# Kernel optimization log

Hardware: AMD Instinct MI355X
Metric: run time of the kernel (lower is better)

## Reference

```python
import jax, jax.numpy as jnp
import numpy as np

N = 100000        # nodes
E = 3200000       # edges (avg in-degree ~32)
NG = 64           # graphs in batch
F_IN = 64         # num_node_features
AVG_LOG = float(np.log(33.0))   # avg log-degree baked from deg (avg degree 32)
BN_EPS = 1e-5
STD_EPS = 1e-5

def _glorot(key, fi, fo):
    lim = float(np.sqrt(6.0 / (fi + fo)))
    return jax.random.uniform(key, (fi, fo), jnp.float32, -lim, lim)

def setup_inputs():
    key = jax.random.key(0)
    ks = jax.random.split(key, 16)
    inp = {
        'x': jax.random.normal(ks[0], (N, F_IN), jnp.float32),
        'edge_index': jax.random.randint(ks[1], (2, E), 0, N),
        'batch': jnp.sort(jax.random.randint(ks[2], (N,), 0, NG)),
    }
    dims = [(F_IN, 96), (96, 64), (64, 32), (32, 20)]
    for i, (fi, fo) in enumerate(dims):
        inp[f'w{i}'] = _glorot(ks[3 + i], 13 * fi, fo)  # (4 aggr * 3 scalers + 1 self) * F_in
        inp[f'b{i}'] = jnp.zeros((fo,), jnp.float32)
    for i, c in enumerate([96, 64, 20]):
        inp[f'g{i}'] = jnp.ones((c,), jnp.float32)
        inp[f'be{i}'] = jnp.zeros((c,), jnp.float32)
    inp['w_lin'] = _glorot(ks[10], 20, 11)
    inp['b_lin'] = jnp.zeros((11,), jnp.float32)
    return inp

def _pna_layer(x, src, dst, cnt, degc, W, b):
    m = x[src]                                          # [E, F] gather of neighbor feats
    inv = (1.0 / degc)[:, None]
    mean = jax.ops.segment_sum(m, dst, N) * inv
    mean_sq = jax.ops.segment_sum(m * m, dst, N) * inv
    std = jnp.sqrt(jax.nn.relu(mean_sq - mean * mean) + STD_EPS)
    has = (cnt > 0)[:, None]
    mn = jnp.where(has, jax.ops.segment_min(m, dst, N), 0.0)
    mx = jnp.where(has, jax.ops.segment_max(m, dst, N), 0.0)
    agg = jnp.concatenate([mean, mn, mx, std], axis=-1)  # [N, 4F]
    logd = jnp.log(degc + 1.0)[:, None]
    out = jnp.concatenate([agg, agg * (logd / AVG_LOG), agg * (AVG_LOG / logd)], axis=-1)  # [N, 12F]
    out = jnp.concatenate([x, out], axis=-1)             # [N, 13F] self + scaled aggregations
    return out @ W + b

def _bn(x, g, b):
    mu = x.mean(0)
    var = x.var(0)  # biased var: matches torch BatchNorm training forward
    return (x - mu) * jax.lax.rsqrt(var + BN_EPS) * g + b

def _forward(x, edge_index, batch, w0, b0, w1, b1, w2, b2, w3, b3,
             g0, be0, g1, be1, g2, be2, w_lin, b_lin):
    src, dst = edge_index[0], edge_index[1]
    cnt = jax.ops.segment_sum(jnp.ones((E,), x.dtype), dst, N)  # in-degree
    degc = jnp.maximum(cnt, 1.0)
    h = jax.nn.relu(_bn(_pna_layer(x, src, dst, cnt, degc, w0, b0), g0, be0))
    h = jax.nn.relu(_bn(_pna_layer(h, src, dst, cnt, degc, w1, b1), g1, be1))
    h = jax.nn.relu(_pna_layer(h, src, dst, cnt, degc, w2, b2))
    h = _bn(_pna_layer(h, src, dst, cnt, degc, w3, b3), g2, be2)
    gcnt = jnp.maximum(jax.ops.segment_sum(jnp.ones((N,), h.dtype), batch, NG), 1.0)
    z = jax.ops.segment_sum(h, batch, NG) / gcnt[:, None]       # global mean pool [NG, 20]
    out = jax.nn.softmax(z @ w_lin + b_lin, axis=-1)            # dropout identity (eval)
    return out, z

def reference(x, edge_index, batch, w0, b0, w1, b1, w2, b2, w3, b3,
              g0, be0, g1, be1, g2, be2, w_lin, b_lin):
    return _forward(x, edge_index, batch, w0, b0, w1, b1, w2, b2, w3, b3,
                    g0, be0, g1, be1, g2, be2, w_lin, b_lin)
```

## Files before the change

### kernel.cpp

```cpp
#include <hip/hip_runtime.h>

#define NN 100000
#define NGRAPH 64
#define NPART 8
#define NPB 12500
#define DB 16
#define NSB 768
#define AVGLOG 3.4965075614664802f

using f32x4 = __attribute__((ext_vector_type(4))) float;
using f16x8 = __attribute__((ext_vector_type(8))) _Float16;
using f16x4 = __attribute__((ext_vector_type(4))) _Float16;

__global__ __launch_bounds__(256) void k_binstage(
    const int* __restrict__ ei, int* __restrict__ bcur,
    unsigned long long* __restrict__ bkt, int cap, int E) {
  __shared__ unsigned long long s_bkt[NPART][NSB];
  __shared__ int s_cnt[NPART], s_base[NPART];
  const int tid = threadIdx.x;
  const int lane = tid & 63;
  if (tid < NPART) s_cnt[tid] = 0;
  __syncthreads();
  const int total_ch = (E + 511) / 512;
  for (int ch = blockIdx.x; ch < total_ch; ch += gridDim.x) {
    int eA = ch * 512 + tid;
    int eB = eA + 256;
    int bA = -1, bB = -1;
    unsigned long long vA = 0, vB = 0;
    if (eA < E) {
      int d = __builtin_nontemporal_load(&ei[E + eA]);
      int s = __builtin_nontemporal_load(&ei[eA]);
      bA = d / NPB;
      vA = ((unsigned long long)(unsigned)d << 32) | (unsigned)s;
    }
    if (eB < E) {
      int d = __builtin_nontemporal_load(&ei[E + eB]);
      int s = __builtin_nontemporal_load(&ei[eB]);
      bB = d / NPB;
      vB = ((unsigned long long)(unsigned)d << 32) | (unsigned)s;
    }
#pragma unroll
    for (int b0 = 0; b0 < NPART; ++b0) {
      unsigned long long mA = __ballot(bA == b0);
      unsigned long long mB = __ballot(bB == b0);
      int cA = __popcll(mA);
      int tot = cA + __popcll(mB);
      if (tot) {
        int base = 0;
        if (lane == 0) base = atomicAdd(&s_cnt[b0], tot);
        base = __shfl(base, 0);
        if (bA == b0)
          s_bkt[b0][base + __popcll(mA & ((1ull << lane) - 1ull))] = vA;
        if (bB == b0)
          s_bkt[b0][base + cA + __popcll(mB & ((1ull << lane) - 1ull))] = vB;
      }
    }
    __syncthreads();
#pragma unroll
    for (int b0 = 0; b0 < NPART; ++b0) {
      int c = s_cnt[b0];
      int nfl = (c >= 512) ? (c & ~255) : 0;
      if (nfl) {
        if (tid == 0) s_base[b0] = atomicAdd(&bcur[b0], nfl);
        __syncthreads();
        int base = s_base[b0];
        for (int i = tid; i < nfl; i += 256)
          bkt[(size_t)b0 * cap + base + i] = s_bkt[b0][i];
        __syncthreads();
        int rem = c - nfl;
        if (tid < rem) s_bkt[b0][tid] = s_bkt[b0][nfl + tid];
        if (tid == 0) s_cnt[b0] = rem;
        __syncthreads();
      }
    }
  }
#pragma unroll
  for (int b0 = 0; b0 < NPART; ++b0) {
    int c = s_cnt[b0];
    if (c) {
      if (tid == 0) s_base[b0] = atomicAdd(&bcur[b0], c);
      __syncthreads();
      int base = s_base[b0];
      for (int i = tid; i < c; i += 256)
        bkt[(size_t)b0 * cap + base + i] = s_bkt[b0][i];
    }
    __syncthreads();
  }
}

__global__ __launch_bounds__(256) void k_dhist(
    const unsigned long long* __restrict__ bkt, const int* __restrict__ bcur,
    int cap, int* __restrict__ dhist) {
  __shared__ int hist[NPB];
  const int p = blockIdx.x & (NPART - 1);
  const int b = blockIdx.x >> 3;
  const int tid = threadIdx.x;
  for (int i = tid; i < NPB; i += 256) hist[i] = 0;
  __syncthreads();
  const int n = bcur[p];
  const int chunk = (n + DB - 1) / DB;
  const int lo = b * chunk, hi = min(n, lo + chunk);
  const unsigned long long* base = bkt + (size_t)p * cap;
  const int plo = p * NPB;
  for (int i = lo + tid; i < hi; i += 256) {
    unsigned long long v = base[i];
    atomicAdd(&hist[(int)(v >> 32) - plo], 1);
  }
  __syncthreads();
  int* dst = dhist + ((size_t)p * DB + b) * NPB;
  for (int i = tid; i < NPB; i += 256) dst[i] = hist[i];
}

__global__ void k_mergesum(int* __restrict__ dhist, int* __restrict__ cnt,
                           int* __restrict__ bsum, int n) {
  __shared__ int s[256];
  int i = blockIdx.x * 256 + threadIdx.x;
  int acc = 0;
  if (i < n) {
    int p = i / NPB, li = i - p * NPB;
    int* hb = dhist + (size_t)p * DB * NPB + li;
#pragma unroll
    for (int b = 0; b < DB; ++b) {
      int t = hb[b * NPB];
      hb[b * NPB] = acc;
      acc += t;
    }
    cnt[i] = acc;
  }
  s[threadIdx.x] = acc;
  __syncthreads();
  for (int off = 128; off > 0; off >>= 1) {
    if (threadIdx.x < off) s[threadIdx.x] += s[threadIdx.x + off];
    __syncthreads();
  }
  if (threadIdx.x == 0) bsum[blockIdx.x] = s[0];
}

__global__ __launch_bounds__(256) void k_binfill(
    const unsigned long long* __restrict__ bkt, const int* __restrict__ bcur,
    int cap, const int* __restrict__ dhist, const int* __restrict__ row_ptr,
    int* __restrict__ colv) {
  __shared__ int rank[NPB];
  const int p = blockIdx.x & (NPART - 1);
  const int b = blockIdx.x >> 3;
  const int tid = threadIdx.x;
  const int plo = p * NPB;
  const int* soff = dhist + ((size_t)p * DB + b) * NPB;
  for (int li = tid; li < NPB; li += 256) rank[li] = row_ptr[plo + li] + soff[li];
  __syncthreads();
  const int n = bcur[p];
  const int chunk = (n + DB - 1) / DB;
  const int lo = b * chunk, hi = min(n, lo + chunk);
  const unsigned long long* base = bkt + (size_t)p * cap;
  for (int i = lo + tid; i < hi; i += 256) {
    unsigned long long v = base[i];
    int d = (int)(v >> 32);
    int s = (int)(v & 0xffffffffu);
    int pos = atomicAdd(&rank[d - plo], 1);
    colv[pos] = s;
  }
}

__global__ void k_scanb(const int* __restrict__ bsum, int* __restrict__ boff, int nb) {
  __shared__ int s[512];
  int t = threadIdx.x;
  int v = (t < nb) ? bsum[t] : 0;
  s[t] = v;
  __syncthreads();
  for (int off = 1; off < 512; off <<= 1) {
    int u = (t >= off) ? s[t - off] : 0;
    __syncthreads();
    s[t] += u;
    __syncthreads();
  }
  if (t < nb) boff[t] = s[t] - v;
}

__global__ void k_scatter(const int* __restrict__ cnt, const int* __restrict__ boff,
                          int* __restrict__ row_ptr, int n, int etot) {
  __shared__ int s[256];
  int i = blockIdx.x * 256 + threadIdx.x;
  int v = (i < n) ? cnt[i] : 0;
  s[threadIdx.x] = v;
  __syncthreads();
  for (int off = 1; off < 256; off <<= 1) {
    int u = (threadIdx.x >= off) ? s[threadIdx.x - off] : 0;
    __syncthreads();
    s[threadIdx.x] += u;
    __syncthreads();
  }
  if (i < n) row_ptr[i] = boff[blockIdx.x] + s[threadIdx.x] - v;
  if (i == 0) row_ptr[n] = etot;
}

__global__ void k_nodesc(const int* __restrict__ cnt, float* __restrict__ invd,
                         float* __restrict__ s1v, float* __restrict__ s2v, int n) {
  int i = blockIdx.x * 256 + threadIdx.x;
  if (i >= n) return;
  float degc = fmaxf((float)cnt[i], 1.f);
  invd[i] = 1.f / degc;
  float ld = logf(degc + 1.f);
  s1v[i] = ld * (1.f / AVGLOG);
  s2v[i] = AVGLOG / ld;
}

__global__ void k_wtprep(const float* __restrict__ W, _Float16* __restrict__ Wt,
                         int K, int FO, int FOP) {
  int i = blockIdx.x * 256 + threadIdx.x;
  if (i >= FOP * K) return;
  int nn = i / K, k = i - nn * K;
  float v = (nn < FO) ? W[k * FO + nn] : 0.f;
  int NT = FOP >> 4;
  int kt = k >> 5, q = (k >> 3) & 3, j = k & 7;
  int nt = nn >> 4, m = nn & 15;
  size_t idx = (((size_t)kt * NT + nt) * 64 + (q * 16 + m)) * 8 + j;
  Wt[idx] = (_Float16)v;
}

__global__ void k_xconv(const float* __restrict__ x, _Float16* __restrict__ x16, int n) {
  int i = blockIdx.x * 256 + threadIdx.x;
  if (i < n) x16[i] = (_Float16)x[i];
}

template <int F, int WPE>
__launch_bounds__(256, WPE)
__global__ void k_agg(const _Float16* __restrict__ hin, const int* __restrict__ row_ptr,
                      const int* __restrict__ colv, const float* __restrict__ invd,
                      _Float16* __restrict__ agg) {
  const int tid = threadIdx.x;
  const int r = tid >> 3, g = tid & 7;
  const int n = blockIdx.x * 32 + r;
  const int e0 = row_ptr[n], e1 = row_ptr[n + 1];
  constexpr int SEG = F / 8;
  constexpr int N8 = (SEG % 8 == 0) ? SEG / 8 : 0;
  constexpr int N4 = (SEG % 8 == 0) ? 0 : SEG / 4;
  constexpr int KTA = F / 8;
  float sm[SEG], sq[SEG], mn[SEG], mx[SEG];
  const float FINF = __builtin_inff();
#pragma unroll
  for (int j = 0; j < SEG; ++j) { sm[j] = 0.f; sq[j] = 0.f; mn[j] = FINF; mx[j] = -FINF; }
  int e = e0;
  for (; e + 1 < e1; e += 2) {
    const _Float16* ra = hin + (size_t)colv[e] * F + g * SEG;
    const _Float16* rb = hin + (size_t)colv[e + 1] * F + g * SEG;
    f16x8 a8[N8 ? N8 : 1], b8[N8 ? N8 : 1];
    f16x4 a4[N4 ? N4 : 1], b4[N4 ? N4 : 1];
    if (N8) {
#pragma unroll
      for (int c = 0; c < N8; ++c) { a8[c] = ((const f16x8*)ra)[c]; b8[c] = ((const f16x8*)rb)[c]; }
    } else {
#pragma unroll
      for (int c = 0; c < N4; ++c) { a4[c] = ((const f16x4*)ra)[c]; b4[c] = ((const f16x4*)rb)[c]; }
    }
#pragma unroll
    for (int j = 0; j < SEG; ++j) {
      float av = N8 ? (float)a8[j / 8][j % 8] : (float)a4[j / 4][j % 4];
      float bv = N8 ? (float)b8[j / 8][j % 8] : (float)b4[j / 4][j % 4];
      sm[j] += av + bv;
      sq[j] += av * av + bv * bv;
      mn[j] = fminf(mn[j], fminf(av, bv));
      mx[j] = fmaxf(mx[j], fmaxf(av, bv));
    }
  }
  if (e < e1) {
    const _Float16* ra = hin + (size_t)colv[e] * F + g * SEG;
    f16x8 a8[N8 ? N8 : 1];
    f16x4 a4[N4 ? N4 : 1];
    if (N8) {
#pragma unroll
      for (int c = 0; c < N8; ++c) a8[c] = ((const f16x8*)ra)[c];
    } else {
#pragma unroll
      for (int c = 0; c < N4; ++c) a4[c] = ((const f16x4*)ra)[c];
    }
#pragma unroll
    for (int j = 0; j < SEG; ++j) {
      float av = N8 ? (float)a8[j / 8][j % 8] : (float)a4[j / 4][j % 4];
      sm[j] += av;
      sq[j] += av * av;
      mn[j] = fminf(mn[j], av);
      mx[j] = fmaxf(mx[j], av);
    }
  }
  float iv = invd[n];
  bool has = (e1 > e0);
  const int m = n & 15;
  const size_t tb = (size_t)(n >> 4) * KTA;
#pragma unroll
  for (int c = 0; c < SEG / 4; ++c) {
    f16x4 vals[4];
#pragma unroll
    for (int l = 0; l < 4; ++l) {
      int j = 4 * c + l;
      float mean = sm[j] * iv;
      float var = sq[j] * iv - mean * mean;
      float sd = sqrtf(fmaxf(var, 0.f) + 1e-5f);
      vals[0][l] = (_Float16)mean;
      vals[1][l] = has ? (_Float16)mn[j] : (_Float16)0.f;
      vals[2][l] = has ? (_Float16)mx[j] : (_Float16)0.f;
      vals[3][l] = (_Float16)sd;
    }
    int f0 = g * SEG + 4 * c;
#pragma unroll
    for (int a = 0; a < 4; ++a) {
      int kk0 = a * F + f0;
      int kt = kk0 >> 5, q = (kk0 >> 3) & 3, j0 = kk0 & 7;
      *(f16x4*)(agg + (tb + kt) * 512 + (q * 16 + m) * 8 + j0) = vals[a];
    }
  }
}

#define MFMA16(a, b, c) __builtin_amdgcn_mfma_f32_16x16x32_f16(a, b, c, 0, 0, 0)

template <int F, int FO, int FOP, bool RELU, bool STATS, typename OT>
__launch_bounds__(256)
__global__ void k_mlp(const _Float16* __restrict__ hin, const _Float16* __restrict__ agg,
                      const float* __restrict__ s1g, const float* __restrict__ s2g,
                      const _Float16* __restrict__ Wt, const float* __restrict__ bias,
                      OT* __restrict__ hout, float* __restrict__ csum,
                      float* __restrict__ csq) {
  constexpr int F32 = F / 32;
  constexpr int KTA = F / 8;
  constexpr int NT = FOP / 16;
  constexpr int PPW = (2 * NT) / 4;
  constexpr int XW = F + 8;
  __shared__ __align__(16) _Float16 s_x[32][XW];
  __shared__ float s_cs[2][FOP];

  const int tid = threadIdx.x;
  const int n0 = blockIdx.x * 32;

  for (int idx = tid; idx < 32 * (F / 8); idx += 256) {
    int r = idx / (F / 8), c = idx % (F / 8);
    *(f16x8*)&s_x[r][8 * c] = *(const f16x8*)&hin[(size_t)(n0 + r) * F + 8 * c];
  }
  if (STATS)
    for (int u = tid; u < 2 * FOP; u += 256) (&s_cs[0][0])[u] = 0.f;
  __syncthreads();

  const int w = tid >> 6, ln = tid & 63;
  const int lm = ln & 15, q = ln >> 4;
  const int mt = w & 1;
  const int arow = mt * 16 + lm;
  f32x4 acc0[PPW], acc1[PPW], acc2[PPW];
#pragma unroll
  for (int i = 0; i < PPW; ++i)
#pragma unroll
    for (int t = 0; t < 4; ++t) { acc0[i][t] = 0.f; acc1[i][t] = 0.f; acc2[i][t] = 0.f; }

#pragma unroll
  for (int kt = 0; kt < F32; ++kt) {
    f16x8 a = *(const f16x8*)&s_x[arow][kt * 32 + 8 * q];
#pragma unroll
    for (int i = 0; i < PPW; ++i) {
      int nt = (w >> 1) + 2 * i;
      f16x8 b = *(const f16x8*)&Wt[(((size_t)kt * NT + nt) * 64 + ln) * 8];
      acc0[i] = MFMA16(a, b, acc0[i]);
    }
  }
  const size_t atb = (size_t)(blockIdx.x * 2 + mt) * KTA;
#pragma unroll
  for (int kt = 0; kt < KTA; ++kt) {
    f16x8 a = *(const f16x8*)&agg[(atb + kt) * 512 + ln * 8];
#pragma unroll
    for (int i = 0; i < PPW; ++i) {
      int nt = (w >> 1) + 2 * i;
      f16x8 b0 = *(const f16x8*)&Wt[(((size_t)(F32 + kt) * NT + nt) * 64 + ln) * 8];
      acc0[i] = MFMA16(a, b0, acc0[i]);
      f16x8 b1 = *(const f16x8*)&Wt[(((size_t)(F32 + KTA + kt) * NT + nt) * 64 + ln) * 8];
      acc1[i] = MFMA16(a, b1, acc1[i]);
      f16x8 b2 = *(const f16x8*)&Wt[(((size_t)(F32 + 2 * KTA + kt) * NT + nt) * 64 + ln) * 8];
      acc2[i] = MFMA16(a, b2, acc2[i]);
    }
  }

  float s1r[4], s2r[4];
#pragma unroll
  for (int t = 0; t < 4; ++t) {
    int node = n0 + mt * 16 + q * 4 + t;
    s1r[t] = s1g[node];
    s2r[t] = s2g[node];
  }
#pragma unroll
  for (int i = 0; i < PPW; ++i) {
    int nt = (w >> 1) + 2 * i;
    int ncol = nt * 16 + lm;
    if (FOP == FO || ncol < FO) {
      float bs = bias[ncol];
      float cs = 0.f, cq = 0.f;
#pragma unroll
      for (int t = 0; t < 4; ++t) {
        int node = n0 + mt * 16 + q * 4 + t;
        float v = acc0[i][t] + s1r[t] * acc1[i][t] + s2r[t] * acc2[i][t] + bs;
        if (RELU) v = fmaxf(v, 0.f);
        hout[(size_t)node * FO + ncol] = (OT)v;
        cs += v;
        cq += v * v;
      }
      if (STATS) {
        atomicAdd(&s_cs[0][ncol], cs);
        atomicAdd(&s_cs[1][ncol], cq);
      }
    }
  }
  if (STATS) {
    __syncthreads();
    if (tid < FO) {
      atomicAdd(&csum[tid], s_cs[0][tid]);
      atomicAdd(&csq[tid], s_cs[1][tid]);
    }
  }
}

__global__ void k_bn16(_Float16* __restrict__ h, const float* __restrict__ csum,
                       const float* __restrict__ csq, const float* __restrict__ gg,
                       const float* __restrict__ be, int n, int fo, int relu) {
  int i = blockIdx.x * 256 + threadIdx.x;
  int total = (n * fo) >> 3;
  if (i >= total) return;
  int c0 = (i << 3) % fo;
  float invn = 1.f / (float)n;
  f16x8 v = *(const f16x8*)&h[(size_t)i << 3];
  f16x8 o;
#pragma unroll
  for (int j = 0; j < 8; ++j) {
    int c = c0 + j;
    float mu = csum[c] * invn;
    float var = csq[c] * invn - mu * mu;
    float rs = rsqrtf(var + 1e-5f);
    float x = ((float)v[j] - mu) * rs * gg[c] + be[c];
    if (relu) x = fmaxf(x, 0.f);
    o[j] = (_Float16)x;
  }
  *(f16x8*)&h[(size_t)i << 3] = o;
}

__global__ void k_bnf(float* __restrict__ h, const float* __restrict__ csum,
                      const float* __restrict__ csq, const float* __restrict__ gg,
                      const float* __restrict__ be, int n, int fo, int relu) {
  int i = blockIdx.x * 256 + threadIdx.x;
  if (i >= n * fo) return;
  int c = i % fo;
  float invn = 1.f / (float)n;
  float mu = csum[c] * invn;
  float var = csq[c] * invn - mu * mu;
  float rs = rsqrtf(var + 1e-5f);
  float v = (h[i] - mu) * rs * gg[c] + be[c];
  if (relu) v = fmaxf(v, 0.f);
  h[i] = v;
}

__global__ void k_pool(const float* __restrict__ h, const int* __restrict__ batch,
                       float* __restrict__ zsum, float* __restrict__ gcnt, int n) {
  __shared__ float sv[NGRAPH * 20];
  __shared__ float sc[NGRAPH];
  int tid = threadIdx.x;
  for (int u = tid; u < NGRAPH * 20; u += 256) sv[u] = 0.f;
  if (tid < NGRAPH) sc[tid] = 0.f;
  __syncthreads();
  int i = blockIdx.x * 256 + tid;
  if (i < n) {
    int g = batch[i];
    atomicAdd(&sc[g], 1.f);
    for (int j = 0; j < 20; ++j) atomicAdd(&sv[g * 20 + j], h[(size_t)i * 20 + j]);
  }
  __syncthreads();
  if (tid < NGRAPH && sc[tid] != 0.f) {
    atomicAdd(&gcnt[tid], sc[tid]);
    for (int j = 0; j < 20; ++j) atomicAdd(&zsum[tid * 20 + j], sv[tid * 20 + j]);
  }
}

__global__ void k_head(const float* __restrict__ zsum, const float* __restrict__ gcnt,
                       const float* __restrict__ wl, const float* __restrict__ bl,
                       float* __restrict__ out) {
  int g = threadIdx.x;
  if (g >= NGRAPH) return;
  float z[20];
  float icg = 1.f / fmaxf(gcnt[g], 1.f);
#pragma unroll
  for (int j = 0; j < 20; ++j) {
    z[j] = zsum[g * 20 + j] * icg;
    out[NGRAPH * 11 + g * 20 + j] = z[j];
  }
  float lo[11];
#pragma unroll
  for (int o = 0; o < 11; ++o) {
    float a = bl[o];
    for (int j = 0; j < 20; ++j) a += z[j] * wl[j * 11 + o];
    lo[o] = a;
  }
  float m = lo[0];
  for (int o = 1; o < 11; ++o) m = fmaxf(m, lo[o]);
  float s = 0.f;
  for (int o = 0; o < 11; ++o) { lo[o] = expf(lo[o] - m); s += lo[o]; }
  float is = 1.f / s;
  for (int o = 0; o < 11; ++o) out[g * 11 + o] = lo[o] * is;
}

static inline char* carve(char*& p, size_t bytes) {
  char* r = p;
  p += (bytes + 255) & ~(size_t)255;
  return r;
}

extern "C" void kernel_launch(void* const* d_in, const int* in_sizes, int n_in,
                              void* d_out, int out_size, void* d_ws, size_t ws_size,
                              hipStream_t stream) {
  const float* x = (const float*)d_in[0];
  const int* ei = (const int*)d_in[1];
  const int* batch = (const int*)d_in[2];
  const float* W0 = (const float*)d_in[3];
  const float* b0 = (const float*)d_in[4];
  const float* W1 = (const float*)d_in[5];
  const float* b1 = (const float*)d_in[6];
  const float* W2 = (const float*)d_in[7];
  const float* b2 = (const float*)d_in[8];
  const float* W3 = (const float*)d_in[9];
  const float* b3 = (const float*)d_in[10];
  const float* g0 = (const float*)d_in[11];
  const float* be0 = (const float*)d_in[12];
  const float* g1 = (const float*)d_in[13];
  const float* be1 = (const float*)d_in[14];
  const float* g2 = (const float*)d_in[15];
  const float* be2 = (const float*)d_in[16];
  const float* wl = (const float*)d_in[17];
  const float* bl = (const float*)d_in[18];
  float* out = (float*)d_out;

  const int E = in_sizes[1] / 2;
  const int NB = (NN + 255) / 256;
  const int BCAP = E / NPART + 65536;

  char* p = (char*)d_ws;
  int* cnt = (int*)carve(p, (size_t)NN * 4);
  int* row_ptr = (int*)carve(p, (size_t)(NN + 1) * 4);
  int* bsum = (int*)carve(p, 2048);
  int* boff = (int*)carve(p, 2048);
  int* bcur = (int*)carve(p, 256);
  int* colv = (int*)carve(p, (size_t)E * 4);
  unsigned long long* bkt = (unsigned long long*)carve(p, (size_t)NPART * BCAP * 8);
  int* dhist = (int*)carve(p, (size_t)NPART * DB * NPB * 4);
  float* invd = (float*)carve(p, (size_t)NN * 4);
  float* s1v = (float*)carve(p, (size_t)NN * 4);
  float* s2v = (float*)carve(p, (size_t)NN * 4);
  _Float16* Wt0 = (_Float16*)carve(p, (size_t)96 * 832 * 2);
  _Float16* Wt1 = (_Float16*)carve(p, (size_t)64 * 1248 * 2);
  _Float16* Wt2 = (_Float16*)carve(p, (size_t)32 * 832 * 2);
  _Float16* Wt3 = (_Float16*)carve(p, (size_t)32 * 416 * 2);
  float* cs = (float*)carve(p, 192 * 4);
  float* csum = cs;
  float* csq = cs + 96;
  float* pacc = (float*)carve(p, (NGRAPH * 20 + NGRAPH) * 4);
  float* zsum = pacc;
  float* gcnt = pacc + NGRAPH * 20;
  _Float16* x16 = (_Float16*)carve(p, (size_t)NN * 64 * 2);
  _Float16* hA16 = (_Float16*)carve(p, (size_t)NN * 96 * 2);
  _Float16* hB16 = (_Float16*)carve(p, (size_t)NN * 96 * 2);
  _Float16* aggb = (_Float16*)carve(p, (size_t)NN * 4 * 96 * 2);
  float* h3 = (float*)x16;

  hipMemsetAsync(bcur, 0, 256, stream);
  hipMemsetAsync(pacc, 0, (NGRAPH * 20 + NGRAPH) * 4, stream);
  k_binstage<<<768, 256, 0, stream>>>(ei, bcur, bkt, BCAP, E);
  k_dhist<<<NPART * DB, 256, 0, stream>>>(bkt, bcur, BCAP, dhist);
  k_mergesum<<<NB, 256, 0, stream>>>(dhist, cnt, bsum, NN);
  k_scanb<<<1, 512, 0, stream>>>(bsum, boff, NB);
  k_scatter<<<NB, 256, 0, stream>>>(cnt, boff, row_ptr, NN, E);
  k_nodesc<<<NB, 256, 0, stream>>>(cnt, invd, s1v, s2v, NN);
  k_binfill<<<NPART * DB, 256, 0, stream>>>(bkt, bcur, BCAP, dhist, row_ptr, colv);

  k_wtprep<<<(96 * 832 + 255) / 256, 256, 0, stream>>>(W0, Wt0, 832, 96, 96);
  k_wtprep<<<(64 * 1248 + 255) / 256, 256, 0, stream>>>(W1, Wt1, 1248, 64, 64);
  k_wtprep<<<(32 * 832 + 255) / 256, 256, 0, stream>>>(W2, Wt2, 832, 32, 32);
  k_wtprep<<<(32 * 416 + 255) / 256, 256, 0, stream>>>(W3, Wt3, 416, 20, 32);
  k_xconv<<<(NN * 64 + 255) / 256, 256, 0, stream>>>(x, x16, NN * 64);

  const int GP = NN / 32;

  hipMemsetAsync(cs, 0, 192 * 4, stream);
  k_agg<64, 6><<<GP, 256, 0, stream>>>(x16, row_ptr, colv, invd, aggb);
  k_mlp<64, 96, 96, false, true, _Float16><<<GP, 256, 0, stream>>>(x16, aggb, s1v, s2v, Wt0, b0, hA16, csum, csq);
  k_bn16<<<(NN * 96 / 8 + 255) / 256, 256, 0, stream>>>(hA16, csum, csq, g0, be0, NN, 96, 1);

  hipMemsetAsync(cs, 0, 192 * 4, stream);
  k_agg<96, 4><<<GP, 256, 0, stream>>>(hA16, row_ptr, colv, invd, aggb);
  k_mlp<96, 64, 64, false, true, _Float16><<<GP, 256, 0, stream>>>(hA16, aggb, s1v, s2v, Wt1, b1, hB16, csum, csq);
  k_bn16<<<(NN * 64 / 8 + 255) / 256, 256, 0, stream>>>(hB16, csum, csq, g1, be1, NN, 64, 1);

  k_agg<64, 6><<<GP, 256, 0, stream>>>(hB16, row_ptr, colv, invd, aggb);
  k_mlp<64, 32, 32, true, false, _Float16><<<GP, 256, 0, stream>>>(hB16, aggb, s1v, s2v, Wt2, b2, hA16, csum, csq);

  hipMemsetAsync(cs, 0, 192 * 4, stream);
  k_agg<32, 8><<<GP, 256, 0, stream>>>(hA16, row_ptr, colv, invd, aggb);
  k_mlp<32, 20, 32, false, true, float><<<GP, 256, 0, stream>>>(hA16, aggb, s1v, s2v, Wt3, b3, h3, csum, csq);
  k_bnf<<<(NN * 20 + 255) / 256, 256, 0, stream>>>(h3, csum, csq, g2, be2, NN, 20, 0);

  k_pool<<<NB, 256, 0, stream>>>(h3, batch, zsum, gcnt, NN);
  k_head<<<1, 64, 0, stream>>>(zsum, gcnt, wl, bl, out);
}
```

Before: 962.7 us.

## Replace partitioned bucket CSR build with direct global-atomic count and fill

Replaces the multi-pass partitioned binning (stage into buckets, per-chunk LDS histograms, merge, LDS-rank fill) with a simpler CSR build. One pass counts in-degree with global atomics, then a scan produces row pointers, then a second pass scatters sources using global atomic ranks. This drops the intermediate 64-bit bucket array and histogram traffic. In exchange it relies on 3.2M contended global atomics, twice, and the column order within a row becomes nondeterministic.

```diff
diff --git a/kernel.cpp b/kernel.cpp
--- a/kernel.cpp
+++ b/kernel.cpp
@@ -2,163 +2,41 @@
 
 #define NN 100000
 #define NGRAPH 64
-#define NPART 8
-#define NPB 12500
-#define DB 16
-#define NSB 768
 #define AVGLOG 3.4965075614664802f
 
 using f32x4 = __attribute__((ext_vector_type(4))) float;
 using f16x8 = __attribute__((ext_vector_type(8))) _Float16;
 using f16x4 = __attribute__((ext_vector_type(4))) _Float16;
-
-__global__ __launch_bounds__(256) void k_binstage(
-    const int* __restrict__ ei, int* __restrict__ bcur,
-    unsigned long long* __restrict__ bkt, int cap, int E) {
-  __shared__ unsigned long long s_bkt[NPART][NSB];
-  __shared__ int s_cnt[NPART], s_base[NPART];
-  const int tid = threadIdx.x;
-  const int lane = tid & 63;
-  if (tid < NPART) s_cnt[tid] = 0;
-  __syncthreads();
-  const int total_ch = (E + 511) / 512;
-  for (int ch = blockIdx.x; ch < total_ch; ch += gridDim.x) {
-    int eA = ch * 512 + tid;
-    int eB = eA + 256;
-    int bA = -1, bB = -1;
-    unsigned long long vA = 0, vB = 0;
-    if (eA < E) {
-      int d = __builtin_nontemporal_load(&ei[E + eA]);
-      int s = __builtin_nontemporal_load(&ei[eA]);
-      bA = d / NPB;
-      vA = ((unsigned long long)(unsigned)d << 32) | (unsigned)s;
-    }
-    if (eB < E) {
-      int d = __builtin_nontemporal_load(&ei[E + eB]);
-      int s = __builtin_nontemporal_load(&ei[eB]);
-      bB = d / NPB;
-      vB = ((unsigned long long)(unsigned)d << 32) | (unsigned)s;
-    }
-#pragma unroll
-    for (int b0 = 0; b0 < NPART; ++b0) {
-      unsigned long long mA = __ballot(bA == b0);
-      unsigned long long mB = __ballot(bB == b0);
-      int cA = __popcll(mA);
-      int tot = cA + __popcll(mB);
-      if (tot) {
-        int base = 0;
-        if (lane == 0) base = atomicAdd(&s_cnt[b0], tot);
-        base = __shfl(base, 0);
-        if (bA == b0)
-          s_bkt[b0][base + __popcll(mA & ((1ull << lane) - 1ull))] = vA;
-        if (bB == b0)
-          s_bkt[b0][base + cA + __popcll(mB & ((1ull << lane) - 1ull))] = vB;
-      }
-    }
-    __syncthreads();
-#pragma unroll
-    for (int b0 = 0; b0 < NPART; ++b0) {
-      int c = s_cnt[b0];
-      int nfl = (c >= 512) ? (c & ~255) : 0;
-      if (nfl) {
-        if (tid == 0) s_base[b0] = atomicAdd(&bcur[b0], nfl);
-        __syncthreads();
-        int base = s_base[b0];
-        for (int i = tid; i < nfl; i += 256)
-          bkt[(size_t)b0 * cap + base + i] = s_bkt[b0][i];
-        __syncthreads();
-        int rem = c - nfl;
-        if (tid < rem) s_bkt[b0][tid] = s_bkt[b0][nfl + tid];
-        if (tid == 0) s_cnt[b0] = rem;
-        __syncthreads();
-      }
-    }
-  }
-#pragma unroll
-  for (int b0 = 0; b0 < NPART; ++b0) {
-    int c = s_cnt[b0];
-    if (c) {
-      if (tid == 0) s_base[b0] = atomicAdd(&bcur[b0], c);
-      __syncthreads();
-      int base = s_base[b0];
-      for (int i = tid; i < c; i += 256)
-        bkt[(size_t)b0 * cap + base + i] = s_bkt[b0][i];
-    }
-    __syncthreads();
-  }
-}
-
-__global__ __launch_bounds__(256) void k_dhist(
-    const unsigned long long* __restrict__ bkt, const int* __restrict__ bcur,
-    int cap, int* __restrict__ dhist) {
-  __shared__ int hist[NPB];
-  const int p = blockIdx.x & (NPART - 1);
-  const int b = blockIdx.x >> 3;
-  const int tid = threadIdx.x;
-  for (int i = tid; i < NPB; i += 256) hist[i] = 0;
-  __syncthreads();
-  const int n = bcur[p];
-  const int chunk = (n + DB - 1) / DB;
-  const int lo = b * chunk, hi = min(n, lo + chunk);
-  const unsigned long long* base = bkt + (size_t)p * cap;
-  const int plo = p * NPB;
-  for (int i = lo + tid; i < hi; i += 256) {
-    unsigned long long v = base[i];
-    atomicAdd(&hist[(int)(v >> 32) - plo], 1);
-  }
-  __syncthreads();
-  int* dst = dhist + ((size_t)p * DB + b) * NPB;
-  for (int i = tid; i < NPB; i += 256) dst[i] = hist[i];
-}
-
-__global__ void k_mergesum(int* __restrict__ dhist, int* __restrict__ cnt,
-                           int* __restrict__ bsum, int n) {
+using i32x4 = __attribute__((ext_vector_type(4))) int;
+
+__global__ __launch_bounds__(256) void k_count(const int* __restrict__ ei,
+                                               int* __restrict__ cnt, int E) {
+  const int n4 = E >> 2;
+  int k = blockIdx.x * 256 + threadIdx.x;
+  if (k < n4) {
+    i32x4 d = __builtin_nontemporal_load(&((const i32x4*)(ei + E))[k]);
+    atomicAdd(&cnt[d[0]], 1);
+    atomicAdd(&cnt[d[1]], 1);
+    atomicAdd(&cnt[d[2]], 1);
+    atomicAdd(&cnt[d[3]], 1);
+  }
+  const int rem = E - (n4 << 2);
+  if (blockIdx.x == 0 && (int)threadIdx.x < rem) {
+    atomicAdd(&cnt[ei[E + (n4 << 2) + threadIdx.x]], 1);
+  }
+}
+
+__global__ void k_bsum(const int* __restrict__ cnt, int* __restrict__ bsum, int n) {
   __shared__ int s[256];
   int i = blockIdx.x * 256 + threadIdx.x;
-  int acc = 0;
-  if (i < n) {
-    int p = i / NPB, li = i - p * NPB;
-    int* hb = dhist + (size_t)p * DB * NPB + li;
-#pragma unroll
-    for (int b = 0; b < DB; ++b) {
-      int t = hb[b * NPB];
-      hb[b * NPB] = acc;
-      acc += t;
-    }
-    cnt[i] = acc;
-  }
-  s[threadIdx.x] = acc;
+  int v = (i < n) ? cnt[i] : 0;
+  s[threadIdx.x] = v;
   __syncthreads();
   for (int off = 128; off > 0; off >>= 1) {
     if (threadIdx.x < off) s[threadIdx.x] += s[threadIdx.x + off];
     __syncthreads();
   }
   if (threadIdx.x == 0) bsum[blockIdx.x] = s[0];
-}
-
-__global__ __launch_bounds__(256) void k_binfill(
-    const unsigned long long* __restrict__ bkt, const int* __restrict__ bcur,
-    int cap, const int* __restrict__ dhist, const int* __restrict__ row_ptr,
-    int* __restrict__ colv) {
-  __shared__ int rank[NPB];
-  const int p = blockIdx.x & (NPART - 1);
-  const int b = blockIdx.x >> 3;
-  const int tid = threadIdx.x;
-  const int plo = p * NPB;
-  const int* soff = dhist + ((size_t)p * DB + b) * NPB;
-  for (int li = tid; li < NPB; li += 256) rank[li] = row_ptr[plo + li] + soff[li];
-  __syncthreads();
-  const int n = bcur[p];
-  const int chunk = (n + DB - 1) / DB;
-  const int lo = b * chunk, hi = min(n, lo + chunk);
-  const unsigned long long* base = bkt + (size_t)p * cap;
-  for (int i = lo + tid; i < hi; i += 256) {
-    unsigned long long v = base[i];
-    int d = (int)(v >> 32);
-    int s = (int)(v & 0xffffffffu);
-    int pos = atomicAdd(&rank[d - plo], 1);
-    colv[pos] = s;
-  }
 }
 
 __global__ void k_scanb(const int* __restrict__ bsum, int* __restrict__ boff, int nb) {
@@ -177,7 +55,8 @@
 }
 
 __global__ void k_scatter(const int* __restrict__ cnt, const int* __restrict__ boff,
-                          int* __restrict__ row_ptr, int n, int etot) {
+                          int* __restrict__ row_ptr, int* __restrict__ rank,
+                          int n, int etot) {
   __shared__ int s[256];
   int i = blockIdx.x * 256 + threadIdx.x;
   int v = (i < n) ? cnt[i] : 0;
@@ -189,8 +68,32 @@
     s[threadIdx.x] += u;
     __syncthreads();
   }
-  if (i < n) row_ptr[i] = boff[blockIdx.x] + s[threadIdx.x] - v;
+  if (i < n) {
+    int rp = boff[blockIdx.x] + s[threadIdx.x] - v;
+    row_ptr[i] = rp;
+    rank[i] = rp;
+  }
   if (i == 0) row_ptr[n] = etot;
+}
+
+__global__ __launch_bounds__(256) void k_fill(const int* __restrict__ ei,
+                                              int* __restrict__ rank,
+                                              int* __restrict__ colv, int E) {
+  const int n4 = E >> 2;
+  int k = blockIdx.x * 256 + threadIdx.x;
+  if (k < n4) {
+    i32x4 s = __builtin_nontemporal_load(&((const i32x4*)ei)[k]);
+    i32x4 d = __builtin_nontemporal_load(&((const i32x4*)(ei + E))[k]);
+    colv[atomicAdd(&rank[d[0]], 1)] = s[0];
+    colv[atomicAdd(&rank[d[1]], 1)] = s[1];
+    colv[atomicAdd(&rank[d[2]], 1)] = s[2];
+    colv[atomicAdd(&rank[d[3]], 1)] = s[3];
+  }
+  const int rem = E - (n4 << 2);
+  if (blockIdx.x == 0 && (int)threadIdx.x < rem) {
+    int e = (n4 << 2) + threadIdx.x;
+    colv[atomicAdd(&rank[ei[E + e]], 1)] = ei[e];
+  }
 }
 
 __global__ void k_nodesc(const int* __restrict__ cnt, float* __restrict__ invd,
@@ -530,17 +433,14 @@
 
   const int E = in_sizes[1] / 2;
   const int NB = (NN + 255) / 256;
-  const int BCAP = E / NPART + 65536;
 
   char* p = (char*)d_ws;
   int* cnt = (int*)carve(p, (size_t)NN * 4);
   int* row_ptr = (int*)carve(p, (size_t)(NN + 1) * 4);
+  int* rank = (int*)carve(p, (size_t)NN * 4);
   int* bsum = (int*)carve(p, 2048);
   int* boff = (int*)carve(p, 2048);
-  int* bcur = (int*)carve(p, 256);
   int* colv = (int*)carve(p, (size_t)E * 4);
-  unsigned long long* bkt = (unsigned long long*)carve(p, (size_t)NPART * BCAP * 8);
-  int* dhist = (int*)carve(p, (size_t)NPART * DB * NPB * 4);
   float* invd = (float*)carve(p, (size_t)NN * 4);
   float* s1v = (float*)carve(p, (size_t)NN * 4);
   float* s2v = (float*)carve(p, (size_t)NN * 4);
@@ -560,15 +460,15 @@
   _Float16* aggb = (_Float16*)carve(p, (size_t)NN * 4 * 96 * 2);
   float* h3 = (float*)x16;
 
-  hipMemsetAsync(bcur, 0, 256, stream);
+  hipMemsetAsync(cnt, 0, (size_t)NN * 4, stream);
   hipMemsetAsync(pacc, 0, (NGRAPH * 20 + NGRAPH) * 4, stream);
-  k_binstage<<<768, 256, 0, stream>>>(ei, bcur, bkt, BCAP, E);
-  k_dhist<<<NPART * DB, 256, 0, stream>>>(bkt, bcur, BCAP, dhist);
-  k_mergesum<<<NB, 256, 0, stream>>>(dhist, cnt, bsum, NN);
+  const int E4B = ((E >> 2) + 255) / 256;
+  k_count<<<E4B, 256, 0, stream>>>(ei, cnt, E);
+  k_bsum<<<NB, 256, 0, stream>>>(cnt, bsum, NN);
   k_scanb<<<1, 512, 0, stream>>>(bsum, boff, NB);
-  k_scatter<<<NB, 256, 0, stream>>>(cnt, boff, row_ptr, NN, E);
+  k_scatter<<<NB, 256, 0, stream>>>(cnt, boff, row_ptr, rank, NN, E);
   k_nodesc<<<NB, 256, 0, stream>>>(cnt, invd, s1v, s2v, NN);
-  k_binfill<<<NPART * DB, 256, 0, stream>>>(bkt, bcur, BCAP, dhist, row_ptr, colv);
+  k_fill<<<E4B, 256, 0, stream>>>(ei, rank, colv, E);
 
   k_wtprep<<<(96 * 832 + 255) / 256, 256, 0, stream>>>(W0, Wt0, 832, 96, 96);
   k_wtprep<<<(64 * 1248 + 255) / 256, 256, 0, stream>>>(W1, Wt1, 1248, 64, 64);
```

New measurement: 1.072 ms. 1.11x slower.

## Replace atomic LDS-staged edge binning with count-scan-scatter partitioning

Applied to the files above, without the earlier changes.

The single-pass binning kernel, which staged edges in shared memory and reserved global space with atomics, is replaced by three kernels. Per-wave partition counts are computed first, then a single-block scan turns them into deterministic base offsets, and a second pass scatters packed edges directly to global buckets using ballot ranks. This drops the shared-memory staging, the block barriers and the global atomics, and loads four edges per lane as vectors. In exchange the edge list is read twice, there are two extra launches, and a serial one-block scan sits between them.

```diff
diff --git a/kernel.cpp b/kernel.cpp
--- a/kernel.cpp
+++ b/kernel.cpp
@@ -5,86 +5,123 @@
 #define NPART 8
 #define NPB 12500
 #define DB 16
-#define NSB 768
+#define PW_C 2048
 #define AVGLOG 3.4965075614664802f
 
 using f32x4 = __attribute__((ext_vector_type(4))) float;
 using f16x8 = __attribute__((ext_vector_type(8))) _Float16;
 using f16x4 = __attribute__((ext_vector_type(4))) _Float16;
-
-__global__ __launch_bounds__(256) void k_binstage(
-    const int* __restrict__ ei, int* __restrict__ bcur,
-    unsigned long long* __restrict__ bkt, int cap, int E) {
-  __shared__ unsigned long long s_bkt[NPART][NSB];
-  __shared__ int s_cnt[NPART], s_base[NPART];
-  const int tid = threadIdx.x;
-  const int lane = tid & 63;
-  if (tid < NPART) s_cnt[tid] = 0;
-  __syncthreads();
-  const int total_ch = (E + 511) / 512;
-  for (int ch = blockIdx.x; ch < total_ch; ch += gridDim.x) {
-    int eA = ch * 512 + tid;
-    int eB = eA + 256;
-    int bA = -1, bB = -1;
-    unsigned long long vA = 0, vB = 0;
-    if (eA < E) {
-      int d = __builtin_nontemporal_load(&ei[E + eA]);
-      int s = __builtin_nontemporal_load(&ei[eA]);
-      bA = d / NPB;
-      vA = ((unsigned long long)(unsigned)d << 32) | (unsigned)s;
-    }
-    if (eB < E) {
-      int d = __builtin_nontemporal_load(&ei[E + eB]);
-      int s = __builtin_nontemporal_load(&ei[eB]);
-      bB = d / NPB;
-      vB = ((unsigned long long)(unsigned)d << 32) | (unsigned)s;
-    }
-#pragma unroll
-    for (int b0 = 0; b0 < NPART; ++b0) {
-      unsigned long long mA = __ballot(bA == b0);
-      unsigned long long mB = __ballot(bB == b0);
-      int cA = __popcll(mA);
-      int tot = cA + __popcll(mB);
-      if (tot) {
-        int base = 0;
-        if (lane == 0) base = atomicAdd(&s_cnt[b0], tot);
-        base = __shfl(base, 0);
-        if (bA == b0)
-          s_bkt[b0][base + __popcll(mA & ((1ull << lane) - 1ull))] = vA;
-        if (bB == b0)
-          s_bkt[b0][base + cA + __popcll(mB & ((1ull << lane) - 1ull))] = vB;
+using i32x4 = __attribute__((ext_vector_type(4))) int;
+
+__global__ __launch_bounds__(256) void k_pcnt(const int* __restrict__ ei,
+                                              int* __restrict__ pcnt, int E, int W) {
+  const int w = blockIdx.x * 4 + (threadIdx.x >> 6);
+  const int lane = threadIdx.x & 63;
+  if (w >= W) return;
+  int c[NPART];
+#pragma unroll
+  for (int b = 0; b < NPART; ++b) c[b] = 0;
+  const long long base = (long long)w * PW_C;
+  for (int r = 0; r < PW_C / 256; ++r) {
+    long long e0 = base + r * 256 + lane * 4;
+    int bk[4] = {-1, -1, -1, -1};
+    if (e0 + 3 < E) {
+      i32x4 d = __builtin_nontemporal_load((const i32x4*)(ei + E + e0));
+#pragma unroll
+      for (int k = 0; k < 4; ++k) bk[k] = d[k] / NPB;
+    } else {
+#pragma unroll
+      for (int k = 0; k < 4; ++k)
+        if (e0 + k < E) bk[k] = ei[E + e0 + k] / NPB;
+    }
+#pragma unroll
+    for (int b = 0; b < NPART; ++b) {
+      int t = 0;
+#pragma unroll
+      for (int k = 0; k < 4; ++k) t += __popcll(__ballot(bk[k] == b));
+      c[b] += t;
+    }
+  }
+  if (lane == 0) {
+#pragma unroll
+    for (int b = 0; b < NPART; ++b) pcnt[w * NPART + b] = c[b];
+  }
+}
+
+__global__ void k_pscan(const int* __restrict__ pcnt, int* __restrict__ pbase,
+                        int* __restrict__ bcur, int W) {
+  __shared__ int s[256];
+  __shared__ int btot[NPART];
+  const int t = threadIdx.x;
+  const int per = (W + 255) / 256;
+  for (int b = 0; b < NPART; ++b) {
+    int loc = 0;
+    const int w0 = t * per;
+    for (int i = 0; i < per; ++i) {
+      int w = w0 + i;
+      if (w < W) loc += pcnt[w * NPART + b];
+    }
+    s[t] = loc;
+    __syncthreads();
+    for (int off = 1; off < 256; off <<= 1) {
+      int u = (t >= off) ? s[t - off] : 0;
+      __syncthreads();
+      s[t] += u;
+      __syncthreads();
+    }
+    int run = s[t] - loc;
+    if (t == 255) btot[b] = s[255];
+    for (int i = 0; i < per; ++i) {
+      int w = w0 + i;
+      if (w < W) {
+        pbase[w * NPART + b] = run;
+        run += pcnt[w * NPART + b];
       }
     }
     __syncthreads();
-#pragma unroll
-    for (int b0 = 0; b0 < NPART; ++b0) {
-      int c = s_cnt[b0];
-      int nfl = (c >= 512) ? (c & ~255) : 0;
-      if (nfl) {
-        if (tid == 0) s_base[b0] = atomicAdd(&bcur[b0], nfl);
-        __syncthreads();
-        int base = s_base[b0];
-        for (int i = tid; i < nfl; i += 256)
-          bkt[(size_t)b0 * cap + base + i] = s_bkt[b0][i];
-        __syncthreads();
-        int rem = c - nfl;
-        if (tid < rem) s_bkt[b0][tid] = s_bkt[b0][nfl + tid];
-        if (tid == 0) s_cnt[b0] = rem;
-        __syncthreads();
+  }
+  if (t < NPART) bcur[t] = btot[t];
+}
+
+__global__ __launch_bounds__(256) void k_pbin(const int* __restrict__ ei,
+                                              const int* __restrict__ pbase,
+                                              unsigned long long* __restrict__ bkt,
+                                              int cap, int E, int W) {
+  const int w = blockIdx.x * 4 + (threadIdx.x >> 6);
+  const int lane = threadIdx.x & 63;
+  if (w >= W) return;
+  int off[NPART];
+#pragma unroll
+  for (int b = 0; b < NPART; ++b) off[b] = pbase[w * NPART + b];
+  const unsigned long long lmask = (1ull << lane) - 1ull;
+  const long long base = (long long)w * PW_C;
+  for (int r = 0; r < PW_C / 256; ++r) {
+    long long e0 = base + r * 256 + lane * 4;
+    int bk[4] = {-1, -1, -1, -1};
+    int sv[4], dv[4];
+    if (e0 + 3 < E) {
+      i32x4 d = __builtin_nontemporal_load((const i32x4*)(ei + E + e0));
+      i32x4 s4 = __builtin_nontemporal_load((const i32x4*)(ei + e0));
+#pragma unroll
+      for (int k = 0; k < 4; ++k) { dv[k] = d[k]; sv[k] = s4[k]; bk[k] = d[k] / NPB; }
+    } else {
+#pragma unroll
+      for (int k = 0; k < 4; ++k)
+        if (e0 + k < E) { dv[k] = ei[E + e0 + k]; sv[k] = ei[e0 + k]; bk[k] = dv[k] / NPB; }
+    }
+#pragma unroll
+    for (int k = 0; k < 4; ++k) {
+#pragma unroll
+      for (int b = 0; b < NPART; ++b) {
+        unsigned long long m = __ballot(bk[k] == b);
+        if (bk[k] == b) {
+          int idx = off[b] + __popcll(m & lmask);
+          bkt[(size_t)b * cap + idx] =
+              ((unsigned long long)(unsigned)dv[k] << 32) | (unsigned)sv[k];
+        }
+        off[b] += __popcll(m);
       }
     }
-  }
-#pragma unroll
-  for (int b0 = 0; b0 < NPART; ++b0) {
-    int c = s_cnt[b0];
-    if (c) {
-      if (tid == 0) s_base[b0] = atomicAdd(&bcur[b0], c);
-      __syncthreads();
-      int base = s_base[b0];
-      for (int i = tid; i < c; i += 256)
-        bkt[(size_t)b0 * cap + base + i] = s_bkt[b0][i];
-    }
-    __syncthreads();
   }
 }
 
@@ -531,6 +568,8 @@
   const int E = in_sizes[1] / 2;
   const int NB = (NN + 255) / 256;
   const int BCAP = E / NPART + 65536;
+  const int W = (E + PW_C - 1) / PW_C;
+  const int GB = (W + 3) / 4;
 
   char* p = (char*)d_ws;
   int* cnt = (int*)carve(p, (size_t)NN * 4);
@@ -538,6 +577,8 @@
   int* bsum = (int*)carve(p, 2048);
   int* boff = (int*)carve(p, 2048);
   int* bcur = (int*)carve(p, 256);
+  int* pcnt = (int*)carve(p, (size_t)W * NPART * 4);
+  int* pbase = (int*)carve(p, (size_t)W * NPART * 4);
   int* colv = (int*)carve(p, (size_t)E * 4);
   unsigned long long* bkt = (unsigned long long*)carve(p, (size_t)NPART * BCAP * 8);
   int* dhist = (int*)carve(p, (size_t)NPART * DB * NPB * 4);
@@ -560,9 +601,10 @@
   _Float16* aggb = (_Float16*)carve(p, (size_t)NN * 4 * 96 * 2);
   float* h3 = (float*)x16;
 
-  hipMemsetAsync(bcur, 0, 256, stream);
   hipMemsetAsync(pacc, 0, (NGRAPH * 20 + NGRAPH) * 4, stream);
-  k_binstage<<<768, 256, 0, stream>>>(ei, bcur, bkt, BCAP, E);
+  k_pcnt<<<GB, 256, 0, stream>>>(ei, pcnt, E, W);
+  k_pscan<<<1, 256, 0, stream>>>(pcnt, pbase, bcur, W);
+  k_pbin<<<GB, 256, 0, stream>>>(ei, pbase, bkt, BCAP, E, W);
   k_dhist<<<NPART * DB, 256, 0, stream>>>(bkt, bcur, BCAP, dhist);
   k_mergesum<<<NB, 256, 0, stream>>>(dhist, cnt, bsum, NN);
   k_scanb<<<1, 512, 0, stream>>>(bsum, boff, NB);
```

New measurement: 895.6 us. 7.0% less time.
